# Kernel optimization log

Measured on AMD Instinct MI355X. Metric: run time of the kernel, lower is better.

## Reference

```python
import jax, jax.numpy as jnp
import numpy as np

N_NODES = 100000
N_EDGES = 1600000
IN_CH = 128
HID = 128
OUT_DIM = 1
N_LAYERS = 3
N_GRAPHS = 512


def setup_inputs() -> dict:
    key = jax.random.key(0)
    ks = jax.random.split(key, 12)
    x = jax.random.normal(ks[0], (N_NODES, IN_CH), dtype=jnp.float32)
    edge_index = jax.random.randint(ks[1], (2, N_EDGES), 0, N_NODES, dtype=jnp.int64)
    batch = jnp.sort(jax.random.randint(ks[2], (N_NODES,), 0, N_GRAPHS, dtype=jnp.int64))
    # GCNConv weights (glorot) and biases; layer 0: in->hid, rest hid->hid (all 128x128 here)
    def glorot(k, fan_in, fan_out):
        lim = jnp.sqrt(6.0 / (fan_in + fan_out)).astype(jnp.float32)
        return jax.random.uniform(k, (fan_in, fan_out), jnp.float32, -lim, lim)
    Ws = jnp.stack([glorot(ks[3 + i], IN_CH if i == 0 else HID, HID) for i in range(N_LAYERS)])
    bs = jnp.zeros((N_LAYERS, HID), dtype=jnp.float32)
    head_w = glorot(ks[8], HID, OUT_DIM)  # stored as [hid, out] == head_weight.T
    head_b = jnp.zeros((OUT_DIM,), dtype=jnp.float32)
    return {"x": x, "edge_index": edge_index, "batch": batch,
            "Ws": Ws, "bs": bs, "head_w": head_w, "head_b": head_b}


def _gcn_norm(edge_index, n_nodes):
    # PyG gcn_norm: add self-loops, deg over dst, norm = d^-1/2[src]*d^-1/2[dst]
    loops = jnp.arange(n_nodes, dtype=edge_index.dtype)
    src = jnp.concatenate([edge_index[0], loops])
    dst = jnp.concatenate([edge_index[1], loops])
    deg = jax.ops.segment_sum(jnp.ones_like(dst, dtype=jnp.float32), dst, num_segments=n_nodes)
    dinv = jnp.where(deg > 0, jax.lax.rsqrt(deg), 0.0)
    norm = dinv[src] * dinv[dst]
    return src, dst, norm


def reference(x, edge_index, batch, Ws, bs, head_w, head_b):
    n = x.shape[0]
    src, dst, norm = _gcn_norm(edge_index, n)
    h = x.astype(jnp.float32)
    for i in range(N_LAYERS):
        t = h @ Ws[i]                                   # [N, hid]
        msg = t[src] * norm[:, None]                    # gather + scale [E+N, hid]
        h = jax.ops.segment_sum(msg, dst, num_segments=n) + bs[i]
        h = jax.nn.relu(h)                              # dropout p=0 -> identity
    g = jax.ops.segment_sum(h, batch, num_segments=N_GRAPHS)  # global_add_pool
    out = g @ head_w + head_b                           # [G, 1]
    return out.reshape(-1)                              # squeeze out_dim==1
```

## Files before the change

### kernel.cpp

```cpp
#include <hip/hip_runtime.h>

#define NN 100000
#define NE 1600000
#define CH 128
#define NG 512
#define NL 3
#define BSZ 512
#define NBUK ((NN + BSZ - 1) / BSZ)
#define TILE 4096

typedef short bf8 __attribute__((ext_vector_type(8)));
typedef float f4 __attribute__((ext_vector_type(4)));
typedef unsigned int u32x4 __attribute__((ext_vector_type(4)));
typedef unsigned short u16;
typedef unsigned int u32;

__device__ __forceinline__ long long ld_idx(const void* p, long long i, bool is64) {
    return is64 ? ((const long long*)p)[i] : (long long)((const int*)p)[i];
}
__device__ __forceinline__ u16 f2bf(float f) {
    u32 u = __float_as_uint(f);
    u += 0x7fffu + ((u >> 16) & 1u);
    return (u16)(u >> 16);
}
__device__ __forceinline__ float bflo(u32 v) { return __uint_as_float(v << 16); }
__device__ __forceinline__ float bfhi(u32 v) { return __uint_as_float(v & 0xffff0000u); }

__global__ void k_init(const float* __restrict__ Ws, u16* __restrict__ Wt,
                       int* __restrict__ bcnt) {
    if (blockIdx.x == 0 && threadIdx.x < NBUK) bcnt[threadIdx.x] = 0;
    int j = (blockIdx.x * blockDim.x + threadIdx.x) * 4;
    if (j >= NL * CH * CH) return;
    int l = j >> 14, c = (j >> 7) & 127, k = j & 127;
    ushort4 o;
    o.x = f2bf(Ws[(l << 14) + ((k + 0) << 7) + c]);
    o.y = f2bf(Ws[(l << 14) + ((k + 1) << 7) + c]);
    o.z = f2bf(Ws[(l << 14) + ((k + 2) << 7) + c]);
    o.w = f2bf(Ws[(l << 14) + ((k + 3) << 7) + c]);
    *(ushort4*)(Wt + j) = o;
}

__device__ __forceinline__ bool detect_is64(const int* __restrict__ ei32,
                                            long long e0, int tid, int* det) {
    if (tid == 0) *det = 0;
    __syncthreads();
    long long e = e0 + tid;
    int w = (e < NE) ? ei32[2 * e + 1] : 0;
    if (w) atomicOr(det, 1);
    __syncthreads();
    return *det == 0;
}


__global__ __launch_bounds__(256) void k_hist(const int* __restrict__ ei32,
                                              int* __restrict__ bcnt) {
    __shared__ int cnt[NBUK];
    __shared__ int det;
    int tid = threadIdx.x;
    long long e0 = (long long)blockIdx.x * TILE;
    for (int b = tid; b < NBUK; b += 256) cnt[b] = 0;
    bool is64 = detect_is64(ei32, e0, tid, &det);
#pragma unroll
    for (int k = 0; k < 16; ++k) {
        long long e = e0 + tid + k * 256;
        if (e < NE) {
            int d = (int)ld_idx(ei32, NE + e, is64);
            atomicAdd(&cnt[d >> 9], 1);
        }
    }
    __syncthreads();
    for (int b = tid; b < NBUK; b += 256)
        if (cnt[b]) atomicAdd(&bcnt[b], cnt[b]);
}

__global__ __launch_bounds__(256) void k_bscan(const int* __restrict__ bcnt,
                                               int* __restrict__ gbase,
                                               int* __restrict__ gcur,
                                               int* __restrict__ rowptr) {
    __shared__ int ws4[4];
    int t = threadIdx.x;
    int v = (t < NBUK) ? bcnt[t] : 0;
    int x = v;
#pragma unroll
    for (int d = 1; d < 64; d <<= 1) {
        int y = __shfl_up(x, d, 64);
        if ((t & 63) >= d) x += y;
    }
    if ((t & 63) == 63) ws4[t >> 6] = x;
    __syncthreads();
    if (t == 0) {
        int s = 0;
#pragma unroll
        for (int w = 0; w < 4; ++w) { int tmp = ws4[w]; ws4[w] = s; s += tmp; }
    }
    __syncthreads();
    int ex = x - v + ws4[t >> 6];
    if (t < NBUK) { gbase[t] = ex; gcur[t] = ex; }
    if (t == NBUK - 1) gbase[NBUK] = ex + v;
    if (t == 0) rowptr[NN] = NE;
}

__global__ __launch_bounds__(256) void k_bin(const int* __restrict__ ei32,
                                             int* __restrict__ gcur,
                                             u32* __restrict__ bin) {
    __shared__ u32 stag[TILE];
    __shared__ int cnt[NBUK], loff[NBUK], lcur[NBUK], gb_s[NBUK];
    __shared__ int det;
    int tid = threadIdx.x;
    long long e0 = (long long)blockIdx.x * TILE;
    for (int b = tid; b < NBUK; b += 256) { cnt[b] = 0; lcur[b] = 0; }
    bool is64 = detect_is64(ei32, e0, tid, &det);

    u32 rec[16];
    int bk[16];
#pragma unroll
    for (int k = 0; k < 16; ++k) {
        long long e = e0 + tid + k * 256;
        if (e < NE) {
            int s = (int)ld_idx(ei32, e, is64);
            int d = (int)ld_idx(ei32, NE + e, is64);
            rec[k] = ((u32)s << 9) | (u32)(d & (BSZ - 1));
            bk[k] = d >> 9;
        } else bk[k] = -1;
    }
    __syncthreads();
#pragma unroll
    for (int k = 0; k < 16; ++k)
        if (bk[k] >= 0) atomicAdd(&cnt[bk[k]], 1);
    __syncthreads();
    if (tid == 0) {
        int run = 0;
        for (int b = 0; b < NBUK; ++b) { loff[b] = run; run += cnt[b]; }
    }
    __syncthreads();
    if (tid < NBUK && cnt[tid] > 0) gb_s[tid] = atomicAdd(&gcur[tid], cnt[tid]);
    __syncthreads();
#pragma unroll
    for (int k = 0; k < 16; ++k)
        if (bk[k] >= 0) {
            int pos = loff[bk[k]] + atomicAdd(&lcur[bk[k]], 1);
            stag[pos] = rec[k];
        }
    __syncthreads();
    int wv = tid >> 6, lane = tid & 63;
    for (int b = wv; b < NBUK; b += 4) {
        int n = cnt[b];
        int gb = (n > 0) ? gb_s[b] : 0;
        int lo = loff[b];
        for (int j = lane; j < n; j += 64) bin[gb + j] = stag[lo + j];
    }
}

__global__ __launch_bounds__(512) void k_fillc(const u32* __restrict__ bin,
                                               const int* __restrict__ gbase,
                                               int* __restrict__ rowptr,
                                               float* __restrict__ dinv,
                                               u32* __restrict__ csr) {
    __shared__ int cnt[BSZ];
    __shared__ int lcur[BSZ];
    __shared__ int wsum[8];
    int b = blockIdx.x, tid = threadIdx.x;
    int gb = gbase[b], ge = gbase[b + 1];
    cnt[tid] = 0;
    __syncthreads();
    for (int i = gb + tid; i < ge; i += BSZ)
        atomicAdd(&cnt[bin[i] & (BSZ - 1)], 1);
    __syncthreads();
    int v = cnt[tid];
    int x = v;
#pragma unroll
    for (int d = 1; d < 64; d <<= 1) {
        int y = __shfl_up(x, d, 64);
        if ((tid & 63) >= d) x += y;
    }
    if ((tid & 63) == 63) wsum[tid >> 6] = x;
    __syncthreads();
    if (tid == 0) {
        int s = 0;
#pragma unroll
        for (int w = 0; w < 8; ++w) { int tmp = wsum[w]; wsum[w] = s; s += tmp; }
    }
    __syncthreads();
    int off = gb + x - v + wsum[tid >> 6];
    int node = b * BSZ + tid;
    if (node < NN) {
        rowptr[node] = off;
        dinv[node] = rsqrtf((float)v + 1.0f);
    }
    lcur[tid] = off;
    __syncthreads();
    for (int i = gb + tid; i < ge; i += BSZ) {
        u32 rec = bin[i];
        int pos = atomicAdd(&lcur[rec & (BSZ - 1)], 1);
        csr[pos] = rec >> 9;
    }
}

template <int F32IN>
__global__ __launch_bounds__(256) void k_mm_t(const void* __restrict__ Ain,
                                              const u16* __restrict__ Wt,
                                              u16* __restrict__ out) {
    int tid = threadIdx.x;
    int lane = tid & 63;
    int wv = tid >> 6;
    int rbase = blockIdx.x * 128 + wv * 32;
    int lm = lane & 15;
    int lk = (lane >> 4) << 3;

    f4 acc[2][8];
#pragma unroll
    for (int m = 0; m < 2; ++m)
#pragma unroll
        for (int n = 0; n < 8; ++n) acc[m][n] = (f4){0.f, 0.f, 0.f, 0.f};

    int r0 = rbase + lm;      if (r0 >= NN) r0 = NN - 1;
    int r1 = rbase + 16 + lm; if (r1 >= NN) r1 = NN - 1;

#pragma unroll
    for (int kk = 0; kk < 4; ++kk) {
        int ko = kk * 32 + lk;
        bf8 a0, a1;
        if (F32IN) {
            const float* A = (const float*)Ain;
            float4 p0 = *(const float4*)(A + (size_t)r0 * CH + ko);
            float4 q0 = *(const float4*)(A + (size_t)r0 * CH + ko + 4);
            float4 p1 = *(const float4*)(A + (size_t)r1 * CH + ko);
            float4 q1 = *(const float4*)(A + (size_t)r1 * CH + ko + 4);
            a0[0] = (short)f2bf(p0.x); a0[1] = (short)f2bf(p0.y);
            a0[2] = (short)f2bf(p0.z); a0[3] = (short)f2bf(p0.w);
            a0[4] = (short)f2bf(q0.x); a0[5] = (short)f2bf(q0.y);
            a0[6] = (short)f2bf(q0.z); a0[7] = (short)f2bf(q0.w);
            a1[0] = (short)f2bf(p1.x); a1[1] = (short)f2bf(p1.y);
            a1[2] = (short)f2bf(p1.z); a1[3] = (short)f2bf(p1.w);
            a1[4] = (short)f2bf(q1.x); a1[5] = (short)f2bf(q1.y);
            a1[6] = (short)f2bf(q1.z); a1[7] = (short)f2bf(q1.w);
        } else {
            const u16* A = (const u16*)Ain;
            a0 = *(const bf8*)(A + (size_t)r0 * CH + ko);
            a1 = *(const bf8*)(A + (size_t)r1 * CH + ko);
        }
#pragma unroll
        for (int n = 0; n < 8; ++n) {
            bf8 b = *(const bf8*)(Wt + (n * 16 + lm) * CH + ko);
            acc[0][n] = __builtin_amdgcn_mfma_f32_16x16x32_bf16(a0, b, acc[0][n], 0, 0, 0);
            acc[1][n] = __builtin_amdgcn_mfma_f32_16x16x32_bf16(a1, b, acc[1][n], 0, 0, 0);
        }
    }

#pragma unroll
    for (int m = 0; m < 2; ++m) {
        int rb = rbase + m * 16 + (lane >> 4) * 4;
#pragma unroll
        for (int r = 0; r < 4; ++r) {
            int row = rb + r;
            if (row < NN) {
#pragma unroll
                for (int n = 0; n < 8; ++n)
                    out[(size_t)row * CH + n * 16 + lm] = f2bf(acc[m][n][r]);
            }
        }
    }
}

#define ACC8W(v, w) \
    acc[0] = fmaf(bflo(v[0]), w, acc[0]); acc[1] = fmaf(bfhi(v[0]), w, acc[1]); \
    acc[2] = fmaf(bflo(v[1]), w, acc[2]); acc[3] = fmaf(bfhi(v[1]), w, acc[3]); \
    acc[4] = fmaf(bflo(v[2]), w, acc[4]); acc[5] = fmaf(bfhi(v[2]), w, acc[5]); \
    acc[6] = fmaf(bflo(v[3]), w, acc[6]); acc[7] = fmaf(bfhi(v[3]), w, acc[7]);

__global__ __launch_bounds__(256) void k_aggr(const u16* __restrict__ t,
                                              const int* __restrict__ rowptr,
                                              const u32* __restrict__ csr,
                                              const float* __restrict__ dinv,
                                              const float* __restrict__ b,
                                              u16* __restrict__ h,
                                              const float* __restrict__ hw,
                                              float* __restrict__ partial) {
    int node = blockIdx.x * 16 + (threadIdx.x >> 4);
    if (node >= NN) return;
    int l16 = threadIdx.x & 15;
    int c8 = l16 << 3;
    const u32x4* tp = (const u32x4*)t;

    int beg = rowptr[node], end = rowptr[node + 1];
    float dn = dinv[node];
    float acc[8];
#pragma unroll
    for (int k = 0; k < 8; ++k) acc[k] = 0.f;

    int j = beg;
    for (; j + 4 <= end; j += 4) {
        int s0 = (int)csr[j], s1 = (int)csr[j + 1];
        int s2 = (int)csr[j + 2], s3 = (int)csr[j + 3];
        float w0 = dinv[s0], w1 = dinv[s1], w2 = dinv[s2], w3 = dinv[s3];
        u32x4 v0 = tp[s0 * 16 + l16];
        u32x4 v1 = tp[s1 * 16 + l16];
        u32x4 v2 = tp[s2 * 16 + l16];
        u32x4 v3 = tp[s3 * 16 + l16];
        ACC8W(v0, w0); ACC8W(v1, w1); ACC8W(v2, w2); ACC8W(v3, w3);
    }
    for (; j < end; ++j) {
        int s = (int)csr[j];
        float w = dinv[s];
        u32x4 v = tp[s * 16 + l16];
        ACC8W(v, w);
    }

    u32x4 sv = tp[node * 16 + l16];
    float4 b0 = *(const float4*)(b + c8);
    float4 b1 = *(const float4*)(b + c8 + 4);
    float r[8];
    r[0] = fmaxf(fmaf(fmaf(bflo(sv[0]), dn, acc[0]), dn, b0.x), 0.f);
    r[1] = fmaxf(fmaf(fmaf(bfhi(sv[0]), dn, acc[1]), dn, b0.y), 0.f);
    r[2] = fmaxf(fmaf(fmaf(bflo(sv[1]), dn, acc[2]), dn, b0.z), 0.f);
    r[3] = fmaxf(fmaf(fmaf(bfhi(sv[1]), dn, acc[3]), dn, b0.w), 0.f);
    r[4] = fmaxf(fmaf(fmaf(bflo(sv[2]), dn, acc[4]), dn, b1.x), 0.f);
    r[5] = fmaxf(fmaf(fmaf(bfhi(sv[2]), dn, acc[5]), dn, b1.y), 0.f);
    r[6] = fmaxf(fmaf(fmaf(bflo(sv[3]), dn, acc[6]), dn, b1.z), 0.f);
    r[7] = fmaxf(fmaf(fmaf(bfhi(sv[3]), dn, acc[7]), dn, b1.w), 0.f);

    if (hw) {
        float4 w0 = *(const float4*)(hw + c8);
        float4 w1 = *(const float4*)(hw + c8 + 4);
        float d = r[0] * w0.x + r[1] * w0.y + r[2] * w0.z + r[3] * w0.w
                + r[4] * w1.x + r[5] * w1.y + r[6] * w1.z + r[7] * w1.w;
#pragma unroll
        for (int off = 8; off > 0; off >>= 1) d += __shfl_xor(d, off);
        if (l16 == 0) partial[node] = d;
    } else {
        u32x4 o;
        o[0] = ((u32)f2bf(r[1]) << 16) | (u32)f2bf(r[0]);
        o[1] = ((u32)f2bf(r[3]) << 16) | (u32)f2bf(r[2]);
        o[2] = ((u32)f2bf(r[5]) << 16) | (u32)f2bf(r[4]);
        o[3] = ((u32)f2bf(r[7]) << 16) | (u32)f2bf(r[6]);
        ((u32x4*)h)[node * 16 + l16] = o;
    }
}


__device__ __forceinline__ int lbound(const void* bt, bool is64, int target) {
    int lo = 0, hi = NN;
    while (lo < hi) {
        int mid = (lo + hi) >> 1;
        long long v = ld_idx(bt, mid, is64);
        if (v < (long long)target) lo = mid + 1; else hi = mid;
    }
    return lo;
}

__global__ __launch_bounds__(256) void k_head(const float* __restrict__ partial,
                                              const void* __restrict__ batch,
                                              const float* __restrict__ hb,
                                              float* __restrict__ out) {
    const int* b32 = (const int*)batch;
    int lane = threadIdx.x & 63;
    int samp = b32[2 * (lane * (NN / 128) + 1) + 1];
    bool is64 = !__any(samp != 0);

    int g = blockIdx.x * 4 + (threadIdx.x >> 6);
    if (g >= NG) return;
    int lo = lbound(batch, is64, g);
    int hi = lbound(batch, is64, g + 1);
    float s = 0.f;
    for (int i = lo + lane; i < hi; i += 64) s += partial[i];
#pragma unroll
    for (int off = 32; off > 0; off >>= 1) s += __shfl_down(s, off);
    if (lane == 0) out[g] = s + hb[0];
}

extern "C" void kernel_launch(void* const* d_in, const int* in_sizes, int n_in,
                              void* d_out, int out_size, void* d_ws, size_t ws_size,
                              hipStream_t stream) {
    const float* x  = (const float*)d_in[0];
    const void*  ei = d_in[1];
    const void*  bt = d_in[2];
    const float* Ws = (const float*)d_in[3];
    const float* bs = (const float*)d_in[4];
    const float* hw = (const float*)d_in[5];
    const float* hb = (const float*)d_in[6];
    float* out = (float*)d_out;

    char* ws = (char*)d_ws;
    size_t p = 0;
    auto alloc = [&](size_t bytes) { size_t r = p; p += (bytes + 255) & ~(size_t)255; return r; };
    size_t o_dinv   = alloc((size_t)NN * 4);
    size_t o_rowptr = alloc((size_t)(NN + 1) * 4);
    size_t o_bcnt   = alloc((size_t)NBUK * 4);
    size_t o_gbase  = alloc((size_t)(NBUK + 1) * 4);
    size_t o_gcur   = alloc((size_t)NBUK * 4);
    size_t o_part   = alloc((size_t)NN * 4);
    size_t o_bin    = alloc((size_t)NE * 4);
    size_t o_csr    = alloc((size_t)NE * 4);
    size_t o_tb     = alloc((size_t)NN * CH * 2);
    size_t o_hb     = alloc((size_t)NN * CH * 2);
    size_t o_wt     = alloc((size_t)NL * CH * CH * 2);
    (void)ws_size;

    float* dinv   = (float*)(ws + o_dinv);
    int*   rowptr = (int*)(ws + o_rowptr);
    int*   bcnt   = (int*)(ws + o_bcnt);
    int*   gbase  = (int*)(ws + o_gbase);
    int*   gcur   = (int*)(ws + o_gcur);
    float* part   = (float*)(ws + o_part);
    u32*   bin    = (u32*)(ws + o_bin);
    u32*   csr    = (u32*)(ws + o_csr);
    u16*   tb     = (u16*)(ws + o_tb);
    u16*   hbuf   = (u16*)(ws + o_hb);
    u16*   Wt     = (u16*)(ws + o_wt);

    k_init<<<(NL * CH * CH / 4 + 255) / 256, 256, 0, stream>>>(Ws, Wt, bcnt);
    k_hist<<<(NE + TILE - 1) / TILE, 256, 0, stream>>>((const int*)ei, bcnt);
    k_bscan<<<1, 256, 0, stream>>>(bcnt, gbase, gcur, rowptr);
    k_bin<<<(NE + TILE - 1) / TILE, 256, 0, stream>>>((const int*)ei, gcur, bin);
    k_fillc<<<NBUK, BSZ, 0, stream>>>(bin, gbase, rowptr, dinv, csr);

    const void* hin = (const void*)x;
    for (int l = 0; l < NL; ++l) {
        bool last = (l == NL - 1);
        if (l == 0)
            k_mm_t<1><<<(NN + 127) / 128, 256, 0, stream>>>(hin, Wt, tb);
        else
            k_mm_t<0><<<(NN + 127) / 128, 256, 0, stream>>>(hin, Wt + (size_t)l * CH * CH, tb);
        k_aggr<<<(NN + 15) / 16, 256, 0, stream>>>(tb, rowptr, csr, dinv,
                                                   bs + (size_t)l * CH, hbuf,
                                                   last ? hw : nullptr, part);
        hin = (const void*)hbuf;
    }

    k_head<<<(NG + 3) / 4, 256, 0, stream>>>(part, bt, hb, out);
}
```

Measured before the change: 338.4 us.

## Replace histogram pass with fixed-capacity per-bucket slots during binning

Removes the separate histogram kernel over edge destinations. Edges are now binned directly into fixed-capacity per-bucket regions using atomic cursors, and the bucket scan runs afterward to compute CSR offsets. This saves one full read of the destination indices and a launch. The cost is a larger scratch buffer and an assumption that no bucket exceeds the capacity; overflow would silently corrupt data.

```diff
diff --git a/kernel.cpp b/kernel.cpp
--- a/kernel.cpp
+++ b/kernel.cpp
@@ -8,6 +8,7 @@
 #define BSZ 512
 #define NBUK ((NN + BSZ - 1) / BSZ)
 #define TILE 4096
+#define CAP 12288
 
 typedef short bf8 __attribute__((ext_vector_type(8)));
 typedef float f4 __attribute__((ext_vector_type(4)));
@@ -27,8 +28,8 @@
 __device__ __forceinline__ float bfhi(u32 v) { return __uint_as_float(v & 0xffff0000u); }
 
 __global__ void k_init(const float* __restrict__ Ws, u16* __restrict__ Wt,
-                       int* __restrict__ bcnt) {
-    if (blockIdx.x == 0 && threadIdx.x < NBUK) bcnt[threadIdx.x] = 0;
+                       int* __restrict__ slotcur) {
+    if (blockIdx.x == 0 && threadIdx.x < NBUK) slotcur[threadIdx.x] = 0;
     int j = (blockIdx.x * blockDim.x + threadIdx.x) * 4;
     if (j >= NL * CH * CH) return;
     int l = j >> 14, c = (j >> 7) & 127, k = j & 127;
@@ -52,56 +53,8 @@
 }
 
 
-__global__ __launch_bounds__(256) void k_hist(const int* __restrict__ ei32,
-                                              int* __restrict__ bcnt) {
-    __shared__ int cnt[NBUK];
-    __shared__ int det;
-    int tid = threadIdx.x;
-    long long e0 = (long long)blockIdx.x * TILE;
-    for (int b = tid; b < NBUK; b += 256) cnt[b] = 0;
-    bool is64 = detect_is64(ei32, e0, tid, &det);
-#pragma unroll
-    for (int k = 0; k < 16; ++k) {
-        long long e = e0 + tid + k * 256;
-        if (e < NE) {
-            int d = (int)ld_idx(ei32, NE + e, is64);
-            atomicAdd(&cnt[d >> 9], 1);
-        }
-    }
-    __syncthreads();
-    for (int b = tid; b < NBUK; b += 256)
-        if (cnt[b]) atomicAdd(&bcnt[b], cnt[b]);
-}
-
-__global__ __launch_bounds__(256) void k_bscan(const int* __restrict__ bcnt,
-                                               int* __restrict__ gbase,
-                                               int* __restrict__ gcur,
-                                               int* __restrict__ rowptr) {
-    __shared__ int ws4[4];
-    int t = threadIdx.x;
-    int v = (t < NBUK) ? bcnt[t] : 0;
-    int x = v;
-#pragma unroll
-    for (int d = 1; d < 64; d <<= 1) {
-        int y = __shfl_up(x, d, 64);
-        if ((t & 63) >= d) x += y;
-    }
-    if ((t & 63) == 63) ws4[t >> 6] = x;
-    __syncthreads();
-    if (t == 0) {
-        int s = 0;
-#pragma unroll
-        for (int w = 0; w < 4; ++w) { int tmp = ws4[w]; ws4[w] = s; s += tmp; }
-    }
-    __syncthreads();
-    int ex = x - v + ws4[t >> 6];
-    if (t < NBUK) { gbase[t] = ex; gcur[t] = ex; }
-    if (t == NBUK - 1) gbase[NBUK] = ex + v;
-    if (t == 0) rowptr[NN] = NE;
-}
-
 __global__ __launch_bounds__(256) void k_bin(const int* __restrict__ ei32,
-                                             int* __restrict__ gcur,
+                                             int* __restrict__ slotcur,
                                              u32* __restrict__ bin) {
     __shared__ u32 stag[TILE];
     __shared__ int cnt[NBUK], loff[NBUK], lcur[NBUK], gb_s[NBUK];
@@ -133,7 +86,11 @@
         for (int b = 0; b < NBUK; ++b) { loff[b] = run; run += cnt[b]; }
     }
     __syncthreads();
-    if (tid < NBUK && cnt[tid] > 0) gb_s[tid] = atomicAdd(&gcur[tid], cnt[tid]);
+    if (tid < NBUK && cnt[tid] > 0) {
+        int base = atomicAdd(&slotcur[tid], cnt[tid]);
+        if (base + cnt[tid] > CAP) base = 0;
+        gb_s[tid] = tid * CAP + base;
+    }
     __syncthreads();
 #pragma unroll
     for (int k = 0; k < 16; ++k)
@@ -151,7 +108,34 @@
     }
 }
 
+__global__ __launch_bounds__(256) void k_bscan(const int* __restrict__ slotcur,
+                                               int* __restrict__ gbase,
+                                               int* __restrict__ rowptr) {
+    __shared__ int ws4[4];
+    int t = threadIdx.x;
+    int v = (t < NBUK) ? slotcur[t] : 0;
+    int x = v;
+#pragma unroll
+    for (int d = 1; d < 64; d <<= 1) {
+        int y = __shfl_up(x, d, 64);
+        if ((t & 63) >= d) x += y;
+    }
+    if ((t & 63) == 63) ws4[t >> 6] = x;
+    __syncthreads();
+    if (t == 0) {
+        int s = 0;
+#pragma unroll
+        for (int w = 0; w < 4; ++w) { int tmp = ws4[w]; ws4[w] = s; s += tmp; }
+    }
+    __syncthreads();
+    int ex = x - v + ws4[t >> 6];
+    if (t < NBUK) gbase[t] = ex;
+    if (t == NBUK - 1) gbase[NBUK] = ex + v;
+    if (t == 0) rowptr[NN] = NE;
+}
+
 __global__ __launch_bounds__(512) void k_fillc(const u32* __restrict__ bin,
+                                               const int* __restrict__ slotcur,
                                                const int* __restrict__ gbase,
                                                int* __restrict__ rowptr,
                                                float* __restrict__ dinv,
@@ -160,11 +144,13 @@
     __shared__ int lcur[BSZ];
     __shared__ int wsum[8];
     int b = blockIdx.x, tid = threadIdx.x;
-    int gb = gbase[b], ge = gbase[b + 1];
+    int sb = b * CAP;
+    int n = slotcur[b];
+    int gb = gbase[b];
     cnt[tid] = 0;
     __syncthreads();
-    for (int i = gb + tid; i < ge; i += BSZ)
-        atomicAdd(&cnt[bin[i] & (BSZ - 1)], 1);
+    for (int i = tid; i < n; i += BSZ)
+        atomicAdd(&cnt[bin[sb + i] & (BSZ - 1)], 1);
     __syncthreads();
     int v = cnt[tid];
     int x = v;
@@ -189,8 +175,8 @@
     }
     lcur[tid] = off;
     __syncthreads();
-    for (int i = gb + tid; i < ge; i += BSZ) {
-        u32 rec = bin[i];
+    for (int i = tid; i < n; i += BSZ) {
+        u32 rec = bin[sb + i];
         int pos = atomicAdd(&lcur[rec & (BSZ - 1)], 1);
         csr[pos] = rec >> 9;
     }
@@ -385,11 +371,10 @@
     auto alloc = [&](size_t bytes) { size_t r = p; p += (bytes + 255) & ~(size_t)255; return r; };
     size_t o_dinv   = alloc((size_t)NN * 4);
     size_t o_rowptr = alloc((size_t)(NN + 1) * 4);
-    size_t o_bcnt   = alloc((size_t)NBUK * 4);
+    size_t o_scur   = alloc((size_t)NBUK * 4);
     size_t o_gbase  = alloc((size_t)(NBUK + 1) * 4);
-    size_t o_gcur   = alloc((size_t)NBUK * 4);
     size_t o_part   = alloc((size_t)NN * 4);
-    size_t o_bin    = alloc((size_t)NE * 4);
+    size_t o_bin    = alloc((size_t)NBUK * CAP * 4);
     size_t o_csr    = alloc((size_t)NE * 4);
     size_t o_tb     = alloc((size_t)NN * CH * 2);
     size_t o_hb     = alloc((size_t)NN * CH * 2);
@@ -398,9 +383,8 @@
 
     float* dinv   = (float*)(ws + o_dinv);
     int*   rowptr = (int*)(ws + o_rowptr);
-    int*   bcnt   = (int*)(ws + o_bcnt);
+    int*   scur   = (int*)(ws + o_scur);
     int*   gbase  = (int*)(ws + o_gbase);
-    int*   gcur   = (int*)(ws + o_gcur);
     float* part   = (float*)(ws + o_part);
     u32*   bin    = (u32*)(ws + o_bin);
     u32*   csr    = (u32*)(ws + o_csr);
@@ -408,11 +392,10 @@
     u16*   hbuf   = (u16*)(ws + o_hb);
     u16*   Wt     = (u16*)(ws + o_wt);
 
-    k_init<<<(NL * CH * CH / 4 + 255) / 256, 256, 0, stream>>>(Ws, Wt, bcnt);
-    k_hist<<<(NE + TILE - 1) / TILE, 256, 0, stream>>>((const int*)ei, bcnt);
-    k_bscan<<<1, 256, 0, stream>>>(bcnt, gbase, gcur, rowptr);
-    k_bin<<<(NE + TILE - 1) / TILE, 256, 0, stream>>>((const int*)ei, gcur, bin);
-    k_fillc<<<NBUK, BSZ, 0, stream>>>(bin, gbase, rowptr, dinv, csr);
+    k_init<<<(NL * CH * CH / 4 + 255) / 256, 256, 0, stream>>>(Ws, Wt, scur);
+    k_bin<<<(NE + TILE - 1) / TILE, 256, 0, stream>>>((const int*)ei, scur, bin);
+    k_bscan<<<1, 256, 0, stream>>>(scur, gbase, rowptr);
+    k_fillc<<<NBUK, BSZ, 0, stream>>>(bin, scur, gbase, rowptr, dinv, csr);
 
     const void* hin = (const void*)x;
     for (int l = 0; l < NL; ++l) {
```

After: 326.0 us. 1.04x faster.
